# Kernel tuning notes

Hardware: AMD Instinct MI355X
Metric: run time of the kernel (lower is better)

## Reference

```python
import jax, jax.numpy as jnp
import numpy as np

B = 16384  # batch
D = 64     # input_size (number of causal nodes)
H = 64     # hidden_size of each per-node MLP


def setup_inputs() -> dict:
    key = jax.random.key(0)
    k1, k2, k3 = jax.random.split(key, 3)
    inputs = jax.random.normal(k1, (B, D), dtype=jnp.float32)
    adjacency = jnp.ones((D, D), dtype=jnp.float32)  # buffer initialized to ones
    # stacked per-node weights: net_i = Linear(D->H, no bias) -> ReLU -> Linear(H->1, no bias)
    W1 = jax.random.normal(k2, (D, H, D), dtype=jnp.float32) * (1.0 / np.sqrt(D))
    W2 = jax.random.normal(k3, (D, H), dtype=jnp.float32) * (1.0 / np.sqrt(H))
    return {"inputs": inputs, "adjacency": adjacency, "W1": W1, "W2": W2}


def reference(inputs, adjacency, W1, W2):
    # inputs: [B, D]; adjacency: [D, D]; W1: [D, H, D]; W2: [D, H]
    # Original: repeat inputs to [B, D, D], mask rows by adjacency, then for each
    # node i apply its tiny MLP to row i and concat the scalar outputs -> [B, D].
    masked = inputs[:, None, :] * adjacency[None, :, :]          # [B, D, D]
    h = jax.nn.relu(jnp.einsum('bid,ihd->bih', masked, W1))      # [B, D, H]
    out = jnp.einsum('bih,ih->bi', h, W2)                        # [B, D]
    return out
```

## Files before the change

### kernel.cpp

```cpp
#include <hip/hip_runtime.h>
#include <hip/hip_bf16.h>

constexpr int BN = 16384;
constexpr int DN = 64;
constexpr int HN = 64;
constexpr int W1ELEMS = DN * HN * DN;
constexpr int WCH = W1ELEMS / 4;

typedef __attribute__((ext_vector_type(8))) short short8;
typedef __attribute__((ext_vector_type(4))) float f32x4;
typedef __attribute__((ext_vector_type(2))) float f32x2;

__device__ __forceinline__ unsigned short f2bf(float f) {
    __hip_bfloat16 h = __float2bfloat16(f);
    return *reinterpret_cast<unsigned short*>(&h);
}

__device__ __forceinline__ short8 cvt8(float4 a, float4 b) {
    short8 r;
    r[0] = (short)f2bf(a.x); r[1] = (short)f2bf(a.y);
    r[2] = (short)f2bf(a.z); r[3] = (short)f2bf(a.w);
    r[4] = (short)f2bf(b.x); r[5] = (short)f2bf(b.y);
    r[6] = (short)f2bf(b.z); r[7] = (short)f2bf(b.w);
    return r;
}

#define DPP_ROR_ADD(x, N)                                                     \
    x += __int_as_float(__builtin_amdgcn_update_dpp(                          \
            0, __float_as_int(x), 0x120 + (N), 0xf, 0xf, false))

__global__ __launch_bounds__(256) void w1prep_kernel(
    const float* __restrict__ W1, const float* __restrict__ adj,
    unsigned short* __restrict__ W1bf)
{
    int c = blockIdx.x * 256 + threadIdx.x;
    int flat = c * 4;
    int i = flat >> 12;
    int d = flat & 63;
    float4 w = reinterpret_cast<const float4*>(W1)[c];
    float4 a = *reinterpret_cast<const float4*>(adj + i * DN + d);
    ushort4 o;
    o.x = f2bf(w.x * a.x); o.y = f2bf(w.y * a.y);
    o.z = f2bf(w.z * a.z); o.w = f2bf(w.w * a.w);
    reinterpret_cast<ushort4*>(W1bf)[c] = o;
}

__global__ __launch_bounds__(256, 3) void mlp_kernel(
    const float* __restrict__ X,
    const unsigned short* __restrict__ W1bf,
    const float* __restrict__ W2,
    float* __restrict__ out)
{
    const int btile = blockIdx.x & 127;
    const int ng    = blockIdx.x >> 7;
    const int wave  = threadIdx.x >> 6;
    const int lane  = threadIdx.x & 63;
    const int row16 = lane & 15;
    const int quad  = lane >> 4;

    __shared__ unsigned short ldsW1[4 * HN * DN];
    __shared__ float ldsW2[4 * HN];
    __shared__ float lds_out[128][4];

    const int b0 = btile * 128 + wave * 32;
    const float* aBase = X + (size_t)(b0 + row16) * DN + quad * 8;
    short8 afrag[2][2];
#pragma unroll
    for (int mt = 0; mt < 2; ++mt)
#pragma unroll
        for (int kk = 0; kk < 2; ++kk) {
            const float* p = aBase + mt * 16 * DN + kk * 32;
            float4 v0 = *reinterpret_cast<const float4*>(p);
            float4 v1 = *reinterpret_cast<const float4*>(p + 4);
            afrag[mt][kk] = cvt8(v0, v1);
        }

    {
        const unsigned short* gsrc = W1bf + (size_t)ng * (4 * HN * DN);
#pragma unroll
        for (int it = 0; it < 8; ++it) {
            int chunk = it * 256 + threadIdx.x;
            int nl = chunk >> 9;
            int rem = chunk & 511;
            int h = rem >> 3;
            int c = rem & 7;
            short8 v = *reinterpret_cast<const short8*>(gsrc + chunk * 8);
            int elem = nl * 4096 + h * 64 + ((c ^ (h & 7)) << 3);
            *reinterpret_cast<short8*>(&ldsW1[elem]) = v;
        }
        ldsW2[threadIdx.x] = W2[ng * 256 + threadIdx.x];
    }
    __syncthreads();

#pragma unroll
    for (int j = 0; j < 4; ++j) {
        short8 bfrag[2][4];
#pragma unroll
        for (int kk = 0; kk < 2; ++kk)
#pragma unroll
            for (int nt = 0; nt < 4; ++nt) {
                int h = nt * 16 + row16;
                int elem = j * 4096 + h * 64 + (((kk * 4 + quad) ^ (row16 & 7)) << 3);
                bfrag[kk][nt] = *reinterpret_cast<const short8*>(&ldsW1[elem]);
            }

        float w2v[4];
#pragma unroll
        for (int nt = 0; nt < 4; ++nt)
            w2v[nt] = ldsW2[j * 64 + nt * 16 + row16];

        f32x4 acc[2][4];
#pragma unroll
        for (int mt = 0; mt < 2; ++mt)
#pragma unroll
            for (int nt = 0; nt < 4; ++nt)
                acc[mt][nt] = (f32x4){0.f, 0.f, 0.f, 0.f};

#pragma unroll
        for (int kk = 0; kk < 2; ++kk)
#pragma unroll
            for (int nt = 0; nt < 4; ++nt) {
                acc[0][nt] = __builtin_amdgcn_mfma_f32_16x16x32_bf16(afrag[0][kk], bfrag[kk][nt], acc[0][nt], 0, 0, 0);
                acc[1][nt] = __builtin_amdgcn_mfma_f32_16x16x32_bf16(afrag[1][kk], bfrag[kk][nt], acc[1][nt], 0, 0, 0);
            }

#pragma unroll
        for (int mt = 0; mt < 2; ++mt) {
            f32x2 s01 = (f32x2){0.f, 0.f}, s23 = (f32x2){0.f, 0.f};
#pragma unroll
            for (int nt = 0; nt < 4; ++nt) {
                f32x2 m01 = (f32x2){fmaxf(acc[mt][nt][0], 0.f), fmaxf(acc[mt][nt][1], 0.f)};
                f32x2 m23 = (f32x2){fmaxf(acc[mt][nt][2], 0.f), fmaxf(acc[mt][nt][3], 0.f)};
                s01 += m01 * w2v[nt];
                s23 += m23 * w2v[nt];
            }
            float p[4] = {s01[0], s01[1], s23[0], s23[1]};
#pragma unroll
            for (int r = 0; r < 4; ++r) {
                DPP_ROR_ADD(p[r], 8);
                DPP_ROR_ADD(p[r], 4);
                DPP_ROR_ADD(p[r], 2);
                DPP_ROR_ADD(p[r], 1);
            }
            if (row16 < 4)
                lds_out[wave * 32 + mt * 16 + quad * 4 + row16][j] = p[row16];
        }
    }

    __syncthreads();
    if (threadIdx.x < 128) {
        int row = threadIdx.x;
        float4 v = *reinterpret_cast<const float4*>(&lds_out[row][0]);
        *reinterpret_cast<float4*>(out + (size_t)(btile * 128 + row) * DN + ng * 4) = v;
    }
}

extern "C" void kernel_launch(void* const* d_in, const int* in_sizes, int n_in,
                              void* d_out, int out_size, void* d_ws, size_t ws_size,
                              hipStream_t stream) {
    const float* X   = (const float*)d_in[0];
    const float* adj = (const float*)d_in[1];
    const float* W1  = (const float*)d_in[2];
    const float* W2  = (const float*)d_in[3];
    float* out = (float*)d_out;

    unsigned short* W1bf = (unsigned short*)d_ws;

    w1prep_kernel<<<WCH / 256, 256, 0, stream>>>(W1, adj, W1bf);
    mlp_kernel<<<128 * 16, 256, 0, stream>>>(X, W1bf, W2, out);
}
```

Measured before the change: 78.85 us.

## Fuse W1 masking/bf16 conversion into MLP kernel and double batch tile

Removes the separate W1 preprocessing kernel: each block now loads fp32 W1 and adjacency directly, multiplies and converts them to bf16, and writes the result into swizzled LDS. The batch tile per block grows from 128 to 256 rows (64 per wave), so each staged weight slice serves more MFMAs, and the grid order now places node groups innermost. The bf16 conversion uses packed pair conversion. This saves one launch and the global bf16 round trip, at the cost of every block reading fp32 weights (twice the bytes, mostly served from L2), more accumulator registers, and half as many blocks.

```diff
diff --git a/kernel.cpp b/kernel.cpp
--- a/kernel.cpp
+++ b/kernel.cpp
@@ -4,69 +4,76 @@
 constexpr int BN = 16384;
 constexpr int DN = 64;
 constexpr int HN = 64;
-constexpr int W1ELEMS = DN * HN * DN;
-constexpr int WCH = W1ELEMS / 4;
 
 typedef __attribute__((ext_vector_type(8))) short short8;
 typedef __attribute__((ext_vector_type(4))) float f32x4;
 typedef __attribute__((ext_vector_type(2))) float f32x2;
 
-__device__ __forceinline__ unsigned short f2bf(float f) {
-    __hip_bfloat16 h = __float2bfloat16(f);
-    return *reinterpret_cast<unsigned short*>(&h);
+__device__ __forceinline__ unsigned int pk2(float lo, float hi) {
+    __hip_bfloat162 h = __float22bfloat162_rn(make_float2(lo, hi));
+    return *reinterpret_cast<unsigned int*>(&h);
 }
 
 __device__ __forceinline__ short8 cvt8(float4 a, float4 b) {
-    short8 r;
-    r[0] = (short)f2bf(a.x); r[1] = (short)f2bf(a.y);
-    r[2] = (short)f2bf(a.z); r[3] = (short)f2bf(a.w);
-    r[4] = (short)f2bf(b.x); r[5] = (short)f2bf(b.y);
-    r[6] = (short)f2bf(b.z); r[7] = (short)f2bf(b.w);
-    return r;
+    union { unsigned int u[4]; short8 s; } r;
+    r.u[0] = pk2(a.x, a.y); r.u[1] = pk2(a.z, a.w);
+    r.u[2] = pk2(b.x, b.y); r.u[3] = pk2(b.z, b.w);
+    return r.s;
 }
 
 #define DPP_ROR_ADD(x, N)                                                     \
     x += __int_as_float(__builtin_amdgcn_update_dpp(                          \
             0, __float_as_int(x), 0x120 + (N), 0xf, 0xf, false))
 
-__global__ __launch_bounds__(256) void w1prep_kernel(
-    const float* __restrict__ W1, const float* __restrict__ adj,
-    unsigned short* __restrict__ W1bf)
-{
-    int c = blockIdx.x * 256 + threadIdx.x;
-    int flat = c * 4;
-    int i = flat >> 12;
-    int d = flat & 63;
-    float4 w = reinterpret_cast<const float4*>(W1)[c];
-    float4 a = *reinterpret_cast<const float4*>(adj + i * DN + d);
-    ushort4 o;
-    o.x = f2bf(w.x * a.x); o.y = f2bf(w.y * a.y);
-    o.z = f2bf(w.z * a.z); o.w = f2bf(w.w * a.w);
-    reinterpret_cast<ushort4*>(W1bf)[c] = o;
-}
-
 __global__ __launch_bounds__(256, 3) void mlp_kernel(
     const float* __restrict__ X,
-    const unsigned short* __restrict__ W1bf,
+    const float* __restrict__ adj,
+    const float* __restrict__ W1,
     const float* __restrict__ W2,
     float* __restrict__ out)
 {
-    const int btile = blockIdx.x & 127;
-    const int ng    = blockIdx.x >> 7;
-    const int wave  = threadIdx.x >> 6;
-    const int lane  = threadIdx.x & 63;
+    const int ng    = blockIdx.x & 15;
+    const int btile = blockIdx.x >> 4;
+    const int tid   = threadIdx.x;
+    const int wave  = tid >> 6;
+    const int lane  = tid & 63;
     const int row16 = lane & 15;
     const int quad  = lane >> 4;
 
     __shared__ unsigned short ldsW1[4 * HN * DN];
     __shared__ float ldsW2[4 * HN];
-    __shared__ float lds_out[128][4];
+    __shared__ float lds_out[256][4];
 
-    const int b0 = btile * 128 + wave * 32;
+    ldsW2[tid] = W2[ng * 256 + tid];
+
+    {
+        const float* w1src   = W1 + (size_t)ng * (4 * HN * DN);
+        const float* adjbase = adj + (size_t)(ng * 4) * DN;
+#pragma unroll
+        for (int it = 0; it < 8; ++it) {
+            int c  = it * 256 + tid;
+            int flat = c * 8;
+            int nl = flat >> 12;
+            int h  = (flat >> 6) & 63;
+            int d  = flat & 63;
+            float4 w0 = *reinterpret_cast<const float4*>(w1src + flat);
+            float4 w1v = *reinterpret_cast<const float4*>(w1src + flat + 4);
+            float4 a0 = *reinterpret_cast<const float4*>(adjbase + nl * DN + d);
+            float4 a1 = *reinterpret_cast<const float4*>(adjbase + nl * DN + d + 4);
+            float4 m0 = make_float4(w0.x * a0.x, w0.y * a0.y, w0.z * a0.z, w0.w * a0.w);
+            float4 m1 = make_float4(w1v.x * a1.x, w1v.y * a1.y, w1v.z * a1.z, w1v.w * a1.w);
+            short8 v = cvt8(m0, m1);
+            int c8 = d >> 3;
+            int elem = nl * 4096 + h * 64 + ((c8 ^ (h & 7)) << 3);
+            *reinterpret_cast<short8*>(&ldsW1[elem]) = v;
+        }
+    }
+
+    const int b0 = btile * 256 + wave * 64;
     const float* aBase = X + (size_t)(b0 + row16) * DN + quad * 8;
-    short8 afrag[2][2];
+    short8 afrag[4][2];
 #pragma unroll
-    for (int mt = 0; mt < 2; ++mt)
+    for (int mt = 0; mt < 4; ++mt)
 #pragma unroll
         for (int kk = 0; kk < 2; ++kk) {
             const float* p = aBase + mt * 16 * DN + kk * 32;
@@ -75,57 +82,41 @@
             afrag[mt][kk] = cvt8(v0, v1);
         }
 
-    {
-        const unsigned short* gsrc = W1bf + (size_t)ng * (4 * HN * DN);
-#pragma unroll
-        for (int it = 0; it < 8; ++it) {
-            int chunk = it * 256 + threadIdx.x;
-            int nl = chunk >> 9;
-            int rem = chunk & 511;
-            int h = rem >> 3;
-            int c = rem & 7;
-            short8 v = *reinterpret_cast<const short8*>(gsrc + chunk * 8);
-            int elem = nl * 4096 + h * 64 + ((c ^ (h & 7)) << 3);
-            *reinterpret_cast<short8*>(&ldsW1[elem]) = v;
-        }
-        ldsW2[threadIdx.x] = W2[ng * 256 + threadIdx.x];
-    }
     __syncthreads();
 
 #pragma unroll
     for (int j = 0; j < 4; ++j) {
-        short8 bfrag[2][4];
-#pragma unroll
-        for (int kk = 0; kk < 2; ++kk)
-#pragma unroll
-            for (int nt = 0; nt < 4; ++nt) {
-                int h = nt * 16 + row16;
-                int elem = j * 4096 + h * 64 + (((kk * 4 + quad) ^ (row16 & 7)) << 3);
-                bfrag[kk][nt] = *reinterpret_cast<const short8*>(&ldsW1[elem]);
-            }
-
         float w2v[4];
 #pragma unroll
         for (int nt = 0; nt < 4; ++nt)
             w2v[nt] = ldsW2[j * 64 + nt * 16 + row16];
 
-        f32x4 acc[2][4];
+        f32x4 acc[4][4];
 #pragma unroll
-        for (int mt = 0; mt < 2; ++mt)
+        for (int mt = 0; mt < 4; ++mt)
 #pragma unroll
             for (int nt = 0; nt < 4; ++nt)
                 acc[mt][nt] = (f32x4){0.f, 0.f, 0.f, 0.f};
 
 #pragma unroll
-        for (int kk = 0; kk < 2; ++kk)
+        for (int kk = 0; kk < 2; ++kk) {
+            short8 bfrag[4];
 #pragma unroll
             for (int nt = 0; nt < 4; ++nt) {
-                acc[0][nt] = __builtin_amdgcn_mfma_f32_16x16x32_bf16(afrag[0][kk], bfrag[kk][nt], acc[0][nt], 0, 0, 0);
-                acc[1][nt] = __builtin_amdgcn_mfma_f32_16x16x32_bf16(afrag[1][kk], bfrag[kk][nt], acc[1][nt], 0, 0, 0);
+                int h = nt * 16 + row16;
+                int elem = j * 4096 + h * 64 + (((kk * 4 + quad) ^ (row16 & 7)) << 3);
+                bfrag[nt] = *reinterpret_cast<const short8*>(&ldsW1[elem]);
             }
+#pragma unroll
+            for (int nt = 0; nt < 4; ++nt)
+#pragma unroll
+                for (int mt = 0; mt < 4; ++mt)
+                    acc[mt][nt] = __builtin_amdgcn_mfma_f32_16x16x32_bf16(
+                        afrag[mt][kk], bfrag[nt], acc[mt][nt], 0, 0, 0);
+        }
 
 #pragma unroll
-        for (int mt = 0; mt < 2; ++mt) {
+        for (int mt = 0; mt < 4; ++mt) {
             f32x2 s01 = (f32x2){0.f, 0.f}, s23 = (f32x2){0.f, 0.f};
 #pragma unroll
             for (int nt = 0; nt < 4; ++nt) {
@@ -143,15 +134,14 @@
                 DPP_ROR_ADD(p[r], 1);
             }
             if (row16 < 4)
-                lds_out[wave * 32 + mt * 16 + quad * 4 + row16][j] = p[row16];
+                lds_out[wave * 64 + mt * 16 + quad * 4 + row16][j] = p[row16];
         }
     }
 
     __syncthreads();
-    if (threadIdx.x < 128) {
-        int row = threadIdx.x;
-        float4 v = *reinterpret_cast<const float4*>(&lds_out[row][0]);
-        *reinterpret_cast<float4*>(out + (size_t)(btile * 128 + row) * DN + ng * 4) = v;
+    {
+        float4 v = *reinterpret_cast<const float4*>(&lds_out[tid][0]);
+        *reinterpret_cast<float4*>(out + (size_t)(btile * 256 + tid) * DN + ng * 4) = v;
     }
 }
 
@@ -164,8 +154,6 @@
     const float* W2  = (const float*)d_in[3];
     float* out = (float*)d_out;
 
-    unsigned short* W1bf = (unsigned short*)d_ws;
-
-    w1prep_kernel<<<WCH / 256, 256, 0, stream>>>(W1, adj, W1bf);
-    mlp_kernel<<<128 * 16, 256, 0, stream>>>(X, W1bf, W2, out);
+    (void)d_ws; (void)ws_size;
+    mlp_kernel<<<(BN / 256) * 16, 256, 0, stream>>>(X, adj, W1, W2, out);
 }
```

Measured after the change: 80.76 us. +2.4%, slower.
